# Optimization experiments

Hardware: AMD Instinct MI355X
Metric: run time of the kernel (lower is better)

## Reference

```python
import jax, jax.numpy as jnp
import numpy as np

N_NODES = 100000
N_EDGES = 1600000
IN_DIM = 128
LATENT = [128, 128, 16]  # last entry = num classes (logits dim)


def setup_inputs() -> dict:
    key = jax.random.key(0)
    ks = jax.random.split(key, 16)
    inp = {
        "x": jax.random.normal(ks[0], (N_NODES, IN_DIM), dtype=jnp.float32),
        "edge_index": jax.random.randint(ks[1], (2, N_EDGES), 0, N_NODES, dtype=jnp.int64),
        "edge_weight": jax.random.uniform(ks[2], (N_EDGES,), dtype=jnp.float32),
    }
    dims = [IN_DIM] + LATENT
    for i in range(len(LATENT)):
        fan_in = dims[i]
        scale = 1.0 / np.sqrt(fan_in)
        inp[f"W{i}"] = jax.random.uniform(ks[3 + 2 * i], (dims[i], dims[i + 1]), minval=-scale, maxval=scale, dtype=jnp.float32)
        inp[f"b{i}"] = jax.random.uniform(ks[4 + 2 * i], (dims[i + 1],), minval=-scale, maxval=scale, dtype=jnp.float32)
        inp[f"eps{i}"] = jnp.zeros((), dtype=jnp.float32)  # GINConv train_eps init = 0
    return inp


def _gin_layer(x, W, b, eps, src, dst, edge_weight):
    # message: x_j (optionally scaled by edge weight), summed into target nodes
    msg = x[src]
    if edge_weight is not None:
        msg = msg * edge_weight[:, None]
    agg = jax.ops.segment_sum(msg, dst, num_segments=N_NODES)
    h = (1.0 + eps) * x + agg
    return jax.nn.relu(h @ W + b)  # MLP = Linear + ReLU


def _l2_normalize(x, eps=1e-12):
    norm = jnp.linalg.norm(x, axis=-1, keepdims=True)
    return x / jnp.maximum(norm, eps)


def reference(x, edge_index, edge_weight, W0, b0, eps0, W1, b1, eps1, W2, b2, eps2):
    src, dst = edge_index[0], edge_index[1]
    params = [(W0, b0, eps0), (W1, b1, eps1), (W2, b2, eps2)]
    h = x
    # all but last layer: GINConv(with edge_weight) -> l2 normalize -> ReLU
    for (W, b, e) in params[:-1]:
        h = _gin_layer(h, W, b, e, src, dst, edge_weight)
        h = _l2_normalize(h)  # emb_normlize=True
        h = jax.nn.relu(h)
    # last layer: GINConv WITHOUT edge_weight (forward passes only x, edge_index)
    W, b, e = params[-1]
    logits = _gin_layer(h, W, b, e, src, dst, None)
    probs = jax.nn.softmax(logits, axis=-1)
    return (logits, probs)
```

## Files before the change

kernel.cpp:

```cpp
#include <hip/hip_runtime.h>
#include <hip/hip_bf16.h>

#define N_NODES 100000
#define N_EDGES 1600000
#define DIM 128
#define ODIM 16
#define NB 391
#define PCHUNK 3200
#define PBLK 500
#define FCAP 6144

typedef unsigned int uint32;
typedef float f32x4 __attribute__((ext_vector_type(4)));
typedef short bf16x8 __attribute__((ext_vector_type(8)));

static __device__ __forceinline__ float bflo(uint32 p) { return __uint_as_float(p << 16); }
static __device__ __forceinline__ float bfhi(uint32 p) { return __uint_as_float(p & 0xFFFF0000u); }
static __device__ __forceinline__ unsigned short f2bf(float f) {
  __hip_bfloat16 h = __float2bfloat16(f);
  return *reinterpret_cast<unsigned short*>(&h);
}
static __device__ __forceinline__ uint32 pk2bf(float a, float b) {
  return (uint32)f2bf(a) | ((uint32)f2bf(b) << 16);
}

__global__ __launch_bounds__(256) void bucket_hist_kernel(
    const int* __restrict__ dst, int* __restrict__ bcnt) {
  __shared__ int h[NB];
  int tid = threadIdx.x;
  for (int i = tid; i < NB; i += 256) h[i] = 0;
  __syncthreads();
  int e0 = blockIdx.x * PCHUNK;
  for (int i = tid; i < PCHUNK; i += 256) atomicAdd(&h[dst[e0 + i] >> 8], 1);
  __syncthreads();
  for (int i = tid; i < NB; i += 256)
    if (h[i]) atomicAdd(&bcnt[i], h[i]);
}

__global__ __launch_bounds__(512) void bucket_scan_kernel(
    const int* __restrict__ bcnt, int* __restrict__ bbase,
    int* __restrict__ bcur) {
  __shared__ int sc[512];
  int t = threadIdx.x;
  int v = (t < NB) ? bcnt[t] : 0;
  sc[t] = v;
  __syncthreads();
  for (int off = 1; off < 512; off <<= 1) {
    int a = (t >= off) ? sc[t - off] : 0;
    __syncthreads();
    sc[t] += a;
    __syncthreads();
  }
  if (t < NB) {
    int base = sc[t] - v;
    bbase[t] = base;
    bcur[t] = base;
  }
}

__global__ __launch_bounds__(256) void coarse_partition_kernel(
    const int* __restrict__ src, const int* __restrict__ dst,
    const float* __restrict__ ew, int* __restrict__ bcur,
    int2* __restrict__ epack) {
  __shared__ int hist[NB];
  __shared__ int base_a[NB];
  __shared__ int lcur_a[NB];
  __shared__ int gbase_a[NB];
  __shared__ int2 stg[PCHUNK];
  __shared__ int gpos[PCHUNK];

  int tid = threadIdx.x;
  int e0 = blockIdx.x * PCHUNK;

  for (int i = tid; i < NB; i += 256) hist[i] = 0;
  __syncthreads();
  for (int i = tid; i < PCHUNK; i += 256) atomicAdd(&hist[dst[e0 + i] >> 8], 1);
  __syncthreads();

  if (tid < 64) {
    int run = 0;
#pragma unroll
    for (int c = 0; c < 7; c++) {
      int idx = c * 64 + tid;
      int v = (idx < NB) ? hist[idx] : 0;
      int incl = v;
#pragma unroll
      for (int off = 1; off < 64; off <<= 1) {
        int tv = __shfl_up(incl, off, 64);
        if (tid >= off) incl += tv;
      }
      if (idx < NB) base_a[idx] = run + incl - v;
      run += __shfl(incl, 63, 64);
    }
  }
  __syncthreads();
  for (int i = tid; i < NB; i += 256) {
    int c = hist[i];
    gbase_a[i] = (c > 0) ? atomicAdd(&bcur[i], c) : 0;
    lcur_a[i] = base_a[i];
  }
  __syncthreads();

  for (int i = tid; i < PCHUNK; i += 256) {
    int e = e0 + i;
    int s = src[e], d = dst[e];
    float w = ew[e];
    int b = d >> 8;
    int pos = atomicAdd(&lcur_a[b], 1);
    stg[pos] = make_int2(s | ((d & 255) << 20), __float_as_int(w));
    gpos[pos] = gbase_a[b] + (pos - base_a[b]);
  }
  __syncthreads();
  for (int i = tid; i < PCHUNK; i += 256) epack[gpos[i]] = stg[i];
}

__global__ __launch_bounds__(256) void fine_sort_kernel(
    const int* __restrict__ bbase, int2* __restrict__ epack,
    int* __restrict__ row_ptr) {
  __shared__ int2 ebuf[FCAP];
  __shared__ int hist[256];
  __shared__ int sc[256];
  __shared__ int cur[256];
  int tid = threadIdx.x;
  int b = blockIdx.x;
  int node0 = b << 8;
  int lo = bbase[b];
  int hi = (b == NB - 1) ? N_EDGES : bbase[b + 1];
  int n = hi - lo;
  if (n > FCAP) n = FCAP;
  hist[tid] = 0;
  __syncthreads();
  for (int i = tid; i < n; i += 256) {
    int2 e = epack[lo + i];
    ebuf[i] = e;
    atomicAdd(&hist[(e.x >> 20) & 255], 1);
  }
  __syncthreads();
  sc[tid] = hist[tid];
  __syncthreads();
  for (int off = 1; off < 256; off <<= 1) {
    int a = (tid >= off) ? sc[tid - off] : 0;
    __syncthreads();
    sc[tid] += a;
    __syncthreads();
  }
  int rp = lo + sc[tid] - hist[tid];
  if (node0 + tid < N_NODES) row_ptr[node0 + tid] = rp;
  cur[tid] = rp;
  if (b == 0 && tid == 0) row_ptr[N_NODES] = N_EDGES;
  __syncthreads();
  for (int i = tid; i < n; i += 256) {
    int2 e = ebuf[i];
    int pos = atomicAdd(&cur[(e.x >> 20) & 255], 1);
    epack[pos] = make_int2(e.x & 0xFFFFF, e.y);
  }
}

__global__ __launch_bounds__(256) void cast_x_kernel(
    const float2* __restrict__ x2, uint32* __restrict__ Xu) {
  int i = blockIdx.x * 256 + threadIdx.x;
  if (i < N_NODES * (DIM / 2)) {
    float2 v = x2[i];
    Xu[i] = pk2bf(v.x, v.y);
  }
}

__global__ __launch_bounds__(256) void packW128_kernel(
    const float* __restrict__ W, unsigned short* __restrict__ out) {
  int idx = blockIdx.x * 256 + threadIdx.x;
  int j = idx & 7, lane = (idx >> 3) & 63, nt = (idx >> 9) & 7, kc = idx >> 12;
  int k = kc * 32 + (lane >> 4) * 8 + j;
  int n = nt * 16 + (lane & 15);
  out[idx] = f2bf(W[k * DIM + n]);
}

__global__ __launch_bounds__(256) void packW16_kernel(
    const float* __restrict__ W, unsigned short* __restrict__ out) {
  int idx = blockIdx.x * 256 + threadIdx.x;
  if (idx >= 2048) return;
  int j = idx & 7, lane = (idx >> 3) & 63, kc = idx >> 9;
  int k = kc * 32 + (lane >> 4) * 8 + j;
  int n = lane & 15;
  out[idx] = f2bf(W[k * ODIM + n]);
}

__global__ __launch_bounds__(256) void gather_bf16(
    const uint32* __restrict__ hu, const int* __restrict__ row_ptr,
    const int2* __restrict__ ep, uint32* __restrict__ aggu) {
  int lane = threadIdx.x & 63;
  int node = blockIdx.x * 4 + (threadIdx.x >> 6);
  if (node >= N_NODES) return;
  int grp = lane >> 4, l4 = lane & 15;
  int a = row_ptr[node], bnd = row_ptr[node + 1];
  float acc[8];
#pragma unroll
  for (int k = 0; k < 8; k++) acc[k] = 0.f;

  auto acc8 = [&](float wv, const uint4& p) {
    acc[0] = fmaf(wv, bflo(p.x), acc[0]); acc[1] = fmaf(wv, bfhi(p.x), acc[1]);
    acc[2] = fmaf(wv, bflo(p.y), acc[2]); acc[3] = fmaf(wv, bfhi(p.y), acc[3]);
    acc[4] = fmaf(wv, bflo(p.z), acc[4]); acc[5] = fmaf(wv, bfhi(p.z), acc[5]);
    acc[6] = fmaf(wv, bflo(p.w), acc[6]); acc[7] = fmaf(wv, bfhi(p.w), acc[7]);
  };

  int j = a;
#pragma unroll 1
  for (; j + 16 <= bnd; j += 16) {
    int2 e0 = ep[j + grp];
    int2 e1 = ep[j + 4 + grp];
    int2 e2 = ep[j + 8 + grp];
    int2 e3 = ep[j + 12 + grp];
    uint4 p0 = *(const uint4*)(hu + (size_t)e0.x * 64 + l4 * 4);
    uint4 p1 = *(const uint4*)(hu + (size_t)e1.x * 64 + l4 * 4);
    uint4 p2 = *(const uint4*)(hu + (size_t)e2.x * 64 + l4 * 4);
    uint4 p3 = *(const uint4*)(hu + (size_t)e3.x * 64 + l4 * 4);
    acc8(__int_as_float(e0.y), p0);
    acc8(__int_as_float(e1.y), p1);
    acc8(__int_as_float(e2.y), p2);
    acc8(__int_as_float(e3.y), p3);
  }
  if (j + 8 <= bnd) {
    int2 e0 = ep[j + grp];
    int2 e1 = ep[j + 4 + grp];
    uint4 p0 = *(const uint4*)(hu + (size_t)e0.x * 64 + l4 * 4);
    uint4 p1 = *(const uint4*)(hu + (size_t)e1.x * 64 + l4 * 4);
    acc8(__int_as_float(e0.y), p0);
    acc8(__int_as_float(e1.y), p1);
    j += 8;
  }
  if (j + 4 <= bnd) {
    int2 e0 = ep[j + grp];
    uint4 p0 = *(const uint4*)(hu + (size_t)e0.x * 64 + l4 * 4);
    acc8(__int_as_float(e0.y), p0);
    j += 4;
  }
  if (j < bnd) {
    int idx = j + grp;
    int vld = idx < bnd;
    int2 e = ep[vld ? idx : bnd - 1];
    uint4 p = *(const uint4*)(hu + (size_t)e.x * 64 + l4 * 4);
    float wv = vld ? __int_as_float(e.y) : 0.f;
    acc8(wv, p);
  }
#pragma unroll
  for (int k = 0; k < 8; k++) {
    acc[k] += __shfl_xor(acc[k], 16, 64);
    acc[k] += __shfl_xor(acc[k], 32, 64);
  }
  if (lane < 16) {
    uint4 st = {pk2bf(acc[0], acc[1]), pk2bf(acc[2], acc[3]),
                pk2bf(acc[4], acc[5]), pk2bf(acc[6], acc[7])};
    *(uint4*)(aggu + (size_t)node * 64 + l4 * 4) = st;
  }
}

template <int FUSE_PROJ>
__global__ __launch_bounds__(256) void gin_mlp_mfma(
    const uint32* Xu, const uint32* __restrict__ Au,
    const unsigned char* __restrict__ pW, const float* __restrict__ b,
    const float* __restrict__ eps_p, uint32* outH,
    const unsigned char* __restrict__ pW2, float* __restrict__ y) {
  __shared__ __align__(16) unsigned char As[64 * 272];
  int tid = threadIdx.x;
  int node0 = blockIdx.x * 64;
  float epf = 1.0f + *eps_p;

  for (int i = tid; i < 64 * 64; i += 256) {
    int n = i >> 6, fp = i & 63;
    int node = node0 + n;
    int cn = node < N_NODES ? node : N_NODES - 1;
    size_t idx = (size_t)cn * 64 + fp;
    uint32 xv = Xu[idx], av = Au[idx];
    float u0 = fmaf(epf, bflo(xv), bflo(av));
    float u1 = fmaf(epf, bfhi(xv), bfhi(av));
    *(uint32*)(As + n * 272 + fp * 4) = pk2bf(u0, u1);
  }
  __syncthreads();

  int w = tid >> 6, l = tid & 63;
  int m = l & 15, q = l >> 4;

  f32x4 acc[8];
#pragma unroll
  for (int nt = 0; nt < 8; nt++) acc[nt] = (f32x4){0.f, 0.f, 0.f, 0.f};

  const unsigned char* Abase = As + (w * 16 + m) * 272 + q * 16;
#pragma unroll
  for (int kc = 0; kc < 4; kc++) {
    bf16x8 af = *(const bf16x8*)(Abase + kc * 64);
#pragma unroll
    for (int nt = 0; nt < 8; nt++) {
      bf16x8 bfr = *(const bf16x8*)(pW + (size_t)((kc * 8 + nt) * 64 + l) * 16);
      acc[nt] = __builtin_amdgcn_mfma_f32_16x16x32_bf16(af, bfr, acc[nt], 0, 0, 0);
    }
  }

  float ss[4] = {0.f, 0.f, 0.f, 0.f};
#pragma unroll
  for (int nt = 0; nt < 8; nt++) {
    float bj = b[nt * 16 + m];
#pragma unroll
    for (int r = 0; r < 4; r++) {
      float v = fmaxf(acc[nt][r] + bj, 0.0f);
      acc[nt][r] = v;
      ss[r] += v * v;
    }
  }
#pragma unroll
  for (int r = 0; r < 4; r++) {
    float s = ss[r];
    s += __shfl_xor(s, 1, 64);
    s += __shfl_xor(s, 2, 64);
    s += __shfl_xor(s, 4, 64);
    s += __shfl_xor(s, 8, 64);
    ss[r] = 1.0f / fmaxf(sqrtf(s), 1e-12f);
  }
#pragma unroll
  for (int nt = 0; nt < 8; nt++) {
#pragma unroll
    for (int r = 0; r < 4; r++) {
      unsigned short hv = f2bf(acc[nt][r] * ss[r]);
      *(unsigned short*)(As + (w * 16 + q * 4 + r) * 272 + (nt * 16 + m) * 2) = hv;
    }
  }

  if (FUSE_PROJ) {
    f32x4 accy = (f32x4){0.f, 0.f, 0.f, 0.f};
#pragma unroll
    for (int kc = 0; kc < 4; kc++) {
      bf16x8 af = *(const bf16x8*)(Abase + kc * 64);
      bf16x8 bfr = *(const bf16x8*)(pW2 + (size_t)(kc * 64 + l) * 16);
      accy = __builtin_amdgcn_mfma_f32_16x16x32_bf16(af, bfr, accy, 0, 0, 0);
    }
#pragma unroll
    for (int r = 0; r < 4; r++) {
      int orow = node0 + w * 16 + q * 4 + r;
      if (orow < N_NODES) y[(size_t)orow * ODIM + m] = accy[r];
    }
  }

  __syncthreads();
  int rem = N_NODES - node0; if (rem > 64) rem = 64;
  for (int i = tid; i < 1024; i += 256) {
    int row = i >> 4, seg = i & 15;
    if (row < rem) {
      uint4 vv = *(const uint4*)(As + row * 272 + seg * 16);
      *(uint4*)((unsigned char*)outH + (size_t)(node0 + row) * 256 + seg * 16) = vv;
    }
  }
}

__global__ __launch_bounds__(256) void gather16_final_kernel(
    const float* __restrict__ y, const int* __restrict__ row_ptr,
    const int2* __restrict__ ep, const float* __restrict__ b,
    const float* __restrict__ eps_p, float* __restrict__ out_logits,
    float* __restrict__ out_probs) {
  int lane = threadIdx.x & 63;
  int node = blockIdx.x * 4 + (threadIdx.x >> 6);
  if (node >= N_NODES) return;
  int f = lane & 15, eq = lane >> 4;
  int a = row_ptr[node], bnd = row_ptr[node + 1];
  float acc = 0.0f;
  int j = a + eq;
  for (; j + 8 <= bnd; j += 8) {
    int s0 = ep[j].x, s1 = ep[j + 4].x;
    acc += y[(size_t)s0 * ODIM + f] + y[(size_t)s1 * ODIM + f];
  }
  for (; j < bnd; j += 4) acc += y[(size_t)ep[j].x * ODIM + f];
  acc += __shfl_xor(acc, 16, 64);
  acc += __shfl_xor(acc, 32, 64);
  if (eq == 0) {
    float epf = 1.0f + *eps_p;
    size_t idx = (size_t)node * ODIM + f;
    float logit = fmaxf(fmaf(epf, y[idx], acc) + b[f], 0.0f);
    float mx = logit;
#pragma unroll
    for (int mm = 8; mm >= 1; mm >>= 1) mx = fmaxf(mx, __shfl_xor(mx, mm, 16));
    float e = __expf(logit - mx);
    float ssum = e;
#pragma unroll
    for (int mm = 8; mm >= 1; mm >>= 1) ssum += __shfl_xor(ssum, mm, 16);
    out_logits[idx] = logit;
    out_probs[idx] = e / ssum;
  }
}

extern "C" void kernel_launch(void* const* d_in, const int* in_sizes, int n_in,
                              void* d_out, int out_size, void* d_ws, size_t ws_size,
                              hipStream_t stream) {
  const float* x = (const float*)d_in[0];
  const int* ei = (const int*)d_in[1];
  const float* ew = (const float*)d_in[2];
  const float* W0 = (const float*)d_in[3];
  const float* b0 = (const float*)d_in[4];
  const float* e0 = (const float*)d_in[5];
  const float* W1 = (const float*)d_in[6];
  const float* b1 = (const float*)d_in[7];
  const float* e1 = (const float*)d_in[8];
  const float* W2 = (const float*)d_in[9];
  const float* b2 = (const float*)d_in[10];
  const float* e2 = (const float*)d_in[11];
  float* out = (float*)d_out;

  const int* srcp = ei;
  const int* dstp = ei + N_EDGES;

  char* ws = (char*)d_ws;
  size_t off = 0;
  uint32* Agg = (uint32*)(ws + off);  off += (size_t)N_NODES * DIM * 2;
  uint32* Xb  = (uint32*)(ws + off);  off += (size_t)N_NODES * DIM * 2;
  uint32* H   = (uint32*)(ws + off);  off += (size_t)N_NODES * DIM * 2;
  int2* epack = (int2*)(ws + off);    off += (size_t)N_EDGES * 8;
  float* y    = (float*)(ws + off);   off += (size_t)N_NODES * ODIM * 4;
  int* row_ptr = (int*)(ws + off);    off += (size_t)(N_NODES + 16) * 4;
  int* bcnt   = (int*)(ws + off);     off += 2048;
  int* bbase  = (int*)(ws + off);     off += 2048;
  int* bcur   = (int*)(ws + off);     off += 2048;
  unsigned short* pW0 = (unsigned short*)(ws + off); off += 32768;
  unsigned short* pW1 = (unsigned short*)(ws + off); off += 32768;
  unsigned short* pW2 = (unsigned short*)(ws + off); off += 4096;

  cast_x_kernel<<<(N_NODES * (DIM / 2) + 255) / 256, 256, 0, stream>>>(
      (const float2*)x, Xb);
  packW128_kernel<<<64, 256, 0, stream>>>(W0, pW0);
  packW128_kernel<<<64, 256, 0, stream>>>(W1, pW1);
  packW16_kernel<<<8, 256, 0, stream>>>(W2, pW2);

  hipMemsetAsync(bcnt, 0, NB * sizeof(int), stream);
  bucket_hist_kernel<<<PBLK, 256, 0, stream>>>(dstp, bcnt);
  bucket_scan_kernel<<<1, 512, 0, stream>>>(bcnt, bbase, bcur);
  coarse_partition_kernel<<<PBLK, 256, 0, stream>>>(srcp, dstp, ew, bcur, epack);
  fine_sort_kernel<<<NB, 256, 0, stream>>>(bbase, epack, row_ptr);

  int ggrid = (N_NODES + 3) / 4;
  int mgrid = (N_NODES + 63) / 64;

  gather_bf16<<<ggrid, 256, 0, stream>>>(Xb, row_ptr, epack, Agg);
  gin_mlp_mfma<0><<<mgrid, 256, 0, stream>>>(Xb, Agg, (const unsigned char*)pW0,
                                             b0, e0, H, nullptr, nullptr);
  gather_bf16<<<ggrid, 256, 0, stream>>>(H, row_ptr, epack, Agg);
  gin_mlp_mfma<1><<<mgrid, 256, 0, stream>>>(H, Agg, (const unsigned char*)pW1,
                                             b1, e1, H,
                                             (const unsigned char*)pW2, y);
  gather16_final_kernel<<<ggrid, 256, 0, stream>>>(y, row_ptr, epack, b2, e2,
                                                   out, out + (size_t)N_NODES * ODIM);
}
```

Baseline: 394.1 us.

## Fuse prep kernels, vectorize MLP loads, pack gather FMAs, skip dead H store

Merges the x cast, three weight-pack kernels and the bucket-count memset into one prep launch, removing several launches. The MLP kernel's prologue now loads 16-byte vectors of X and Agg instead of 4-byte words. The gather accumulates in float2 vectors so the compiler can emit packed FMAs. The second MLP layer no longer writes H back to global memory, since only its projection y is consumed afterwards.

```diff
diff --git a/kernel.cpp b/kernel.cpp
--- a/kernel.cpp
+++ b/kernel.cpp
@@ -9,8 +9,10 @@
 #define PCHUNK 3200
 #define PBLK 500
 #define FCAP 6144
+#define CAST_BLOCKS 25000
 
 typedef unsigned int uint32;
+typedef float f32x2 __attribute__((ext_vector_type(2)));
 typedef float f32x4 __attribute__((ext_vector_type(4)));
 typedef short bf16x8 __attribute__((ext_vector_type(8)));
 
@@ -22,6 +24,34 @@
 }
 static __device__ __forceinline__ uint32 pk2bf(float a, float b) {
   return (uint32)f2bf(a) | ((uint32)f2bf(b) << 16);
+}
+
+__global__ __launch_bounds__(256) void prep_kernel(
+    const float2* __restrict__ x2, uint32* __restrict__ Xu,
+    const float* __restrict__ W0, const float* __restrict__ W1,
+    const float* __restrict__ W2,
+    unsigned short* __restrict__ pW0, unsigned short* __restrict__ pW1,
+    unsigned short* __restrict__ pW2, int* __restrict__ bcnt) {
+  int b = blockIdx.x;
+  int tid = threadIdx.x;
+  if (b < CAST_BLOCKS) {
+    int i = b * 256 + tid;
+    float2 v = x2[i];
+    Xu[i] = pk2bf(v.x, v.y);
+  } else if (b < CAST_BLOCKS + 128) {
+    int wsel = (b - CAST_BLOCKS) >> 6;
+    int idx = ((b - CAST_BLOCKS) & 63) * 256 + tid;
+    int j = idx & 7, lane = (idx >> 3) & 63, nt = (idx >> 9) & 7, kc = idx >> 12;
+    const float* W = wsel ? W1 : W0;
+    unsigned short* pW = wsel ? pW1 : pW0;
+    pW[idx] = f2bf(W[(kc * 32 + (lane >> 4) * 8 + j) * DIM + nt * 16 + (lane & 15)]);
+  } else if (b < CAST_BLOCKS + 136) {
+    int idx = (b - CAST_BLOCKS - 128) * 256 + tid;
+    int j = idx & 7, lane = (idx >> 3) & 63, kc = idx >> 9;
+    pW2[idx] = f2bf(W2[(kc * 32 + (lane >> 4) * 8 + j) * ODIM + (lane & 15)]);
+  } else {
+    for (int i = tid; i < NB; i += 256) bcnt[i] = 0;
+  }
 }
 
 __global__ __launch_bounds__(256) void bucket_hist_kernel(
@@ -156,34 +186,6 @@
   }
 }
 
-__global__ __launch_bounds__(256) void cast_x_kernel(
-    const float2* __restrict__ x2, uint32* __restrict__ Xu) {
-  int i = blockIdx.x * 256 + threadIdx.x;
-  if (i < N_NODES * (DIM / 2)) {
-    float2 v = x2[i];
-    Xu[i] = pk2bf(v.x, v.y);
-  }
-}
-
-__global__ __launch_bounds__(256) void packW128_kernel(
-    const float* __restrict__ W, unsigned short* __restrict__ out) {
-  int idx = blockIdx.x * 256 + threadIdx.x;
-  int j = idx & 7, lane = (idx >> 3) & 63, nt = (idx >> 9) & 7, kc = idx >> 12;
-  int k = kc * 32 + (lane >> 4) * 8 + j;
-  int n = nt * 16 + (lane & 15);
-  out[idx] = f2bf(W[k * DIM + n]);
-}
-
-__global__ __launch_bounds__(256) void packW16_kernel(
-    const float* __restrict__ W, unsigned short* __restrict__ out) {
-  int idx = blockIdx.x * 256 + threadIdx.x;
-  if (idx >= 2048) return;
-  int j = idx & 7, lane = (idx >> 3) & 63, kc = idx >> 9;
-  int k = kc * 32 + (lane >> 4) * 8 + j;
-  int n = lane & 15;
-  out[idx] = f2bf(W[k * ODIM + n]);
-}
-
 __global__ __launch_bounds__(256) void gather_bf16(
     const uint32* __restrict__ hu, const int* __restrict__ row_ptr,
     const int2* __restrict__ ep, uint32* __restrict__ aggu) {
@@ -192,15 +194,15 @@
   if (node >= N_NODES) return;
   int grp = lane >> 4, l4 = lane & 15;
   int a = row_ptr[node], bnd = row_ptr[node + 1];
-  float acc[8];
-#pragma unroll
-  for (int k = 0; k < 8; k++) acc[k] = 0.f;
+  f32x2 acc2[4];
+#pragma unroll
+  for (int k = 0; k < 4; k++) acc2[k] = (f32x2){0.f, 0.f};
 
   auto acc8 = [&](float wv, const uint4& p) {
-    acc[0] = fmaf(wv, bflo(p.x), acc[0]); acc[1] = fmaf(wv, bfhi(p.x), acc[1]);
-    acc[2] = fmaf(wv, bflo(p.y), acc[2]); acc[3] = fmaf(wv, bfhi(p.y), acc[3]);
-    acc[4] = fmaf(wv, bflo(p.z), acc[4]); acc[5] = fmaf(wv, bfhi(p.z), acc[5]);
-    acc[6] = fmaf(wv, bflo(p.w), acc[6]); acc[7] = fmaf(wv, bfhi(p.w), acc[7]);
+    acc2[0] += (f32x2){bflo(p.x), bfhi(p.x)} * wv;
+    acc2[1] += (f32x2){bflo(p.y), bfhi(p.y)} * wv;
+    acc2[2] += (f32x2){bflo(p.z), bfhi(p.z)} * wv;
+    acc2[3] += (f32x2){bflo(p.w), bfhi(p.w)} * wv;
   };
 
   int j = a;
@@ -243,13 +245,15 @@
     acc8(wv, p);
   }
 #pragma unroll
-  for (int k = 0; k < 8; k++) {
-    acc[k] += __shfl_xor(acc[k], 16, 64);
-    acc[k] += __shfl_xor(acc[k], 32, 64);
+  for (int k = 0; k < 4; k++) {
+    acc2[k].x += __shfl_xor(acc2[k].x, 16, 64);
+    acc2[k].x += __shfl_xor(acc2[k].x, 32, 64);
+    acc2[k].y += __shfl_xor(acc2[k].y, 16, 64);
+    acc2[k].y += __shfl_xor(acc2[k].y, 32, 64);
   }
   if (lane < 16) {
-    uint4 st = {pk2bf(acc[0], acc[1]), pk2bf(acc[2], acc[3]),
-                pk2bf(acc[4], acc[5]), pk2bf(acc[6], acc[7])};
+    uint4 st = {pk2bf(acc2[0].x, acc2[0].y), pk2bf(acc2[1].x, acc2[1].y),
+                pk2bf(acc2[2].x, acc2[2].y), pk2bf(acc2[3].x, acc2[3].y)};
     *(uint4*)(aggu + (size_t)node * 64 + l4 * 4) = st;
   }
 }
@@ -265,15 +269,22 @@
   int node0 = blockIdx.x * 64;
   float epf = 1.0f + *eps_p;
 
-  for (int i = tid; i < 64 * 64; i += 256) {
-    int n = i >> 6, fp = i & 63;
+  const uint4* X4 = (const uint4*)Xu;
+  const uint4* A4 = (const uint4*)Au;
+#pragma unroll
+  for (int c = 0; c < 4; c++) {
+    int t = c * 256 + tid;
+    int n = t >> 4, s = t & 15;
     int node = node0 + n;
     int cn = node < N_NODES ? node : N_NODES - 1;
-    size_t idx = (size_t)cn * 64 + fp;
-    uint32 xv = Xu[idx], av = Au[idx];
-    float u0 = fmaf(epf, bflo(xv), bflo(av));
-    float u1 = fmaf(epf, bfhi(xv), bfhi(av));
-    *(uint32*)(As + n * 272 + fp * 4) = pk2bf(u0, u1);
+    uint4 xv = X4[(size_t)cn * 16 + s];
+    uint4 av = A4[(size_t)cn * 16 + s];
+    uint4 o;
+    o.x = pk2bf(fmaf(epf, bflo(xv.x), bflo(av.x)), fmaf(epf, bfhi(xv.x), bfhi(av.x)));
+    o.y = pk2bf(fmaf(epf, bflo(xv.y), bflo(av.y)), fmaf(epf, bfhi(xv.y), bfhi(av.y)));
+    o.z = pk2bf(fmaf(epf, bflo(xv.z), bflo(av.z)), fmaf(epf, bfhi(xv.z), bfhi(av.z)));
+    o.w = pk2bf(fmaf(epf, bflo(xv.w), bflo(av.w)), fmaf(epf, bfhi(xv.w), bfhi(av.w)));
+    *(uint4*)(As + n * 272 + s * 16) = o;
   }
   __syncthreads();
 
@@ -337,15 +348,15 @@
       int orow = node0 + w * 16 + q * 4 + r;
       if (orow < N_NODES) y[(size_t)orow * ODIM + m] = accy[r];
     }
-  }
-
-  __syncthreads();
-  int rem = N_NODES - node0; if (rem > 64) rem = 64;
-  for (int i = tid; i < 1024; i += 256) {
-    int row = i >> 4, seg = i & 15;
-    if (row < rem) {
-      uint4 vv = *(const uint4*)(As + row * 272 + seg * 16);
-      *(uint4*)((unsigned char*)outH + (size_t)(node0 + row) * 256 + seg * 16) = vv;
+  } else {
+    __syncthreads();
+    int rem = N_NODES - node0; if (rem > 64) rem = 64;
+    for (int i = tid; i < 1024; i += 256) {
+      int row = i >> 4, seg = i & 15;
+      if (row < rem) {
+        uint4 vv = *(const uint4*)(As + row * 272 + seg * 16);
+        *(uint4*)((unsigned char*)outH + (size_t)(node0 + row) * 256 + seg * 16) = vv;
+      }
     }
   }
 }
@@ -420,13 +431,9 @@
   unsigned short* pW1 = (unsigned short*)(ws + off); off += 32768;
   unsigned short* pW2 = (unsigned short*)(ws + off); off += 4096;
 
-  cast_x_kernel<<<(N_NODES * (DIM / 2) + 255) / 256, 256, 0, stream>>>(
-      (const float2*)x, Xb);
-  packW128_kernel<<<64, 256, 0, stream>>>(W0, pW0);
-  packW128_kernel<<<64, 256, 0, stream>>>(W1, pW1);
-  packW16_kernel<<<8, 256, 0, stream>>>(W2, pW2);
-
-  hipMemsetAsync(bcnt, 0, NB * sizeof(int), stream);
+  prep_kernel<<<CAST_BLOCKS + 137, 256, 0, stream>>>(
+      (const float2*)x, Xb, W0, W1, W2, pW0, pW1, pW2, bcnt);
+
   bucket_hist_kernel<<<PBLK, 256, 0, stream>>>(dstp, bcnt);
   bucket_scan_kernel<<<1, 512, 0, stream>>>(bcnt, bbase, bcur);
   coarse_partition_kernel<<<PBLK, 256, 0, stream>>>(srcp, dstp, ew, bcur, epack);
@@ -440,7 +447,7 @@
                                              b0, e0, H, nullptr, nullptr);
   gather_bf16<<<ggrid, 256, 0, stream>>>(H, row_ptr, epack, Agg);
   gin_mlp_mfma<1><<<mgrid, 256, 0, stream>>>(H, Agg, (const unsigned char*)pW1,
-                                             b1, e1, H,
+                                             b1, e1, nullptr,
                                              (const unsigned char*)pW2, y);
   gather16_final_kernel<<<ggrid, 256, 0, stream>>>(y, row_ptr, epack, b2, e2,
                                                    out, out + (size_t)N_NODES * ODIM);
```

Result: faster. 375.6 us (-4.7%).
